# Optimization experiments

Measured on AMD Instinct MI355X. Metric: run time of the kernel, lower is better.

Reference implementation:

```python
import jax, jax.numpy as jnp
import numpy as np

B, S, DM1, DM2, DK, DV = 8, 2048, 768, 768, 64, 64
EPS = 1e-5


def setup_inputs() -> dict:
    key = jax.random.key(0)
    ks = jax.random.split(key, 8)
    s1 = 1.0 / np.sqrt(DM1)
    s2 = 1.0 / np.sqrt(DM2)
    return {
        "x_1": jax.random.normal(ks[0], (B, S, DM1), jnp.float32),
        "x_2": jax.random.normal(ks[1], (B, S, DM2), jnp.float32),
        "Wq": jax.random.uniform(ks[2], (DM1, DK), jnp.float32, -s1, s1),
        "bq": jnp.zeros((DK,), jnp.float32),
        "Wk": jax.random.uniform(ks[3], (DM2, DK), jnp.float32, -s2, s2),
        "bk": jnp.zeros((DK,), jnp.float32),
        "Wv": jax.random.uniform(ks[4], (DM2, DV), jnp.float32, -s2, s2),
        "bv": jnp.zeros((DV,), jnp.float32),
        "gamma": jnp.ones((DV,), jnp.float32),
        "beta": jnp.zeros((DV,), jnp.float32),
    }


def reference(x_1, x_2, Wq, bq, Wk, bk, Wv, bv, gamma, beta):
    q = jnp.einsum("bsd,dk->bsk", x_1, Wq) + bq            # [B,S,DK]
    k = jnp.einsum("bsd,dk->bsk", x_2, Wk) + bk            # [B,S,DK]
    v = jnp.einsum("bsd,dv->bsv", x_2, Wv) + bv            # [B,S,DV]
    scores = jnp.einsum("bqk,bsk->bqs", q, k) / jnp.sqrt(jnp.float32(DK))
    w = jax.nn.softmax(scores, axis=-1)                    # [B,S,S]
    # reverse-weight transform (reverse=True)
    dim = w.shape[1]
    w = (1.0 - w) / (dim - 1)
    attn = jnp.einsum("bqs,bsv->bqv", w, v)                # [B,S,DV]
    mu = jnp.mean(attn, axis=-1, keepdims=True)
    var = jnp.var(attn, axis=-1, keepdims=True)
    out = (attn - mu) * jax.lax.rsqrt(var + EPS) * gamma + beta
    return out
```

## Files before the change

kernel.cpp:

```cpp
#include <hip/hip_runtime.h>
#include <hip/hip_bf16.h>

#define BATCH 8
#define SEQ   2048
#define DM    768
#define DD    64
#define BS (BATCH * SEQ)
#define SCALEQ 0.1803369380478f

typedef __bf16 bf16x8 __attribute__((ext_vector_type(8)));
typedef float  f32x4  __attribute__((ext_vector_type(4)));
typedef short  short8 __attribute__((ext_vector_type(8)));
typedef short  short4v __attribute__((ext_vector_type(4)));

#define MFMA16(a, b, c) __builtin_amdgcn_mfma_f32_16x16x32_bf16((a), (b), (c), 0, 0, 0)

__device__ __forceinline__ short f2bf(float x) {
    unsigned u = __builtin_bit_cast(unsigned, x);
    u = (u + 0x7fffu + ((u >> 16) & 1u)) >> 16;
    return (short)u;
}
__device__ __forceinline__ float bf2f(short s) {
    unsigned u = ((unsigned)(unsigned short)s) << 16;
    return __builtin_bit_cast(float, u);
}
__device__ __forceinline__ bf16x8 cvt8(float4 a, float4 b) {
    bf16x8 r;
    r[0] = (__bf16)a.x; r[1] = (__bf16)a.y; r[2] = (__bf16)a.z; r[3] = (__bf16)a.w;
    r[4] = (__bf16)b.x; r[5] = (__bf16)b.y; r[6] = (__bf16)b.z; r[7] = (__bf16)b.w;
    return r;
}

__global__ void prep_w_kernel(const float* __restrict__ Wq, const float* __restrict__ Wk,
                              const float* __restrict__ Wv, short* __restrict__ Wt,
                              float* __restrict__ C) {
    int idx = blockIdx.x * 256 + threadIdx.x;
    if (idx < BATCH * DD) C[idx] = 0.f;
    if (idx >= 3 * DM * DD) return;
    int m = idx / (DM * DD);
    int r = (idx % (DM * DD)) / DD;
    int c = idx % DD;
    const float* W = (m == 0) ? Wq : (m == 1) ? Wk : Wv;
    float scale = (m == 0) ? SCALEQ : 1.0f;
    Wt[m * DM * DD + c * DM + r] = f2bf(W[r * DD + c] * scale);
}

#define PHK 192
#define RSTR 200
__global__ __launch_bounds__(256) void proj_kernel(
        const float* __restrict__ x1, const float* __restrict__ x2,
        const short* __restrict__ Wt,
        const float* __restrict__ bq, const float* __restrict__ bk,
        const float* __restrict__ bv,
        short* __restrict__ Qs, short* __restrict__ Kb, short* __restrict__ Vtb,
        float* __restrict__ C) {
    __shared__ __align__(16) short wls[2][64 * RSTR];
    const int tid = threadIdx.x, wave = tid >> 6, lane = tid & 63;
    const int quad = lane >> 4, l15 = lane & 15;
    const int kv = blockIdx.x & 1;
    const int r0 = (blockIdx.x >> 1) * 64;
    const float* x = kv ? x2 : x1;
    const short* W0 = Wt + (kv ? (size_t)(DM * DD) : 0);
    const short* W1 = Wt + 2 * (size_t)(DM * DD);

    const int srow = tid >> 2;
    const int skseg = tid & 3;

    const float* xp = x + (size_t)(r0 + wave * 16 + l15) * DM + quad * 8;

    f32x4 acc0[4] = {}, acc1[4] = {};

    float4 cxa = *(const float4*)(xp);
    float4 cxb = *(const float4*)(xp + 4);

    for (int ph = 0; ph < 4; ph++) {
        const int kbase = ph * PHK;
#pragma unroll
        for (int i = 0; i < 6; i++) {
            int kp = skseg + 4 * i;
            bf16x8 w = *(const bf16x8*)(W0 + (size_t)srow * DM + kbase + kp * 8);
            *(bf16x8*)&wls[0][srow * RSTR + kp * 8] = w;
        }
        if (kv) {
#pragma unroll
            for (int i = 0; i < 6; i++) {
                int kp = skseg + 4 * i;
                bf16x8 w = *(const bf16x8*)(W1 + (size_t)srow * DM + kbase + kp * 8);
                *(bf16x8*)&wls[1][srow * RSTR + kp * 8] = w;
            }
        }
        __syncthreads();
#pragma unroll
        for (int st = 0; st < 6; st++) {
            const int k0 = kbase + st * 32;
            float4 nxa, nxb;
            if (k0 + 32 < DM) {
                nxa = *(const float4*)(xp + k0 + 32);
                nxb = *(const float4*)(xp + k0 + 36);
            }
            bf16x8 af = cvt8(cxa, cxb);
#pragma unroll
            for (int tn = 0; tn < 4; tn++) {
                const int lofs = (tn * 16 + l15) * RSTR + (st * 4 + quad) * 8;
                acc0[tn] = MFMA16(af, *(const bf16x8*)&wls[0][lofs], acc0[tn]);
                if (kv)
                    acc1[tn] = MFMA16(af, *(const bf16x8*)&wls[1][lofs], acc1[tn]);
            }
            cxa = nxa; cxb = nxb;
        }
        __syncthreads();
    }

    if (!kv) {
#pragma unroll
        for (int tn = 0; tn < 4; tn++) {
            int v = tn * 16 + l15;
            float bb = bq[v] * SCALEQ;
#pragma unroll
            for (int r = 0; r < 4; r++)
                Qs[(size_t)(r0 + wave * 16 + quad * 4 + r) * DD + v] = f2bf(acc0[tn][r] + bb);
        }
    } else {
#pragma unroll
        for (int tn = 0; tn < 4; tn++) {
            int v = tn * 16 + l15;
            float bb = bk[v];
#pragma unroll
            for (int r = 0; r < 4; r++)
                Kb[(size_t)(r0 + wave * 16 + quad * 4 + r) * DD + v] = f2bf(acc0[tn][r] + bb);
        }
        const int b = r0 / SEQ;
        const int sbase = (r0 % SEQ) + wave * 16 + quad * 4;
#pragma unroll
        for (int tn = 0; tn < 4; tn++) {
            int v = tn * 16 + l15;
            float bb = bv[v];
            short4v pk;
            float cs = 0.f;
#pragma unroll
            for (int r = 0; r < 4; r++) {
                pk[r] = f2bf(acc1[tn][r] + bb);
                cs += bf2f(pk[r]);
            }
            *(short4v*)(Vtb + ((size_t)b * DD + v) * SEQ + sbase) = pk;
            cs += __shfl_xor(cs, 16);
            cs += __shfl_xor(cs, 32);
            if (quad == 0) atomicAdd(&C[b * DD + v], cs);
        }
    }
}

#define PBS 72
__global__ __launch_bounds__(256, 2) void flash_kernel(
        const short* __restrict__ Q, const short* __restrict__ K,
        const short* __restrict__ Vt,
        short* __restrict__ Yp, float* __restrict__ Dp) {
    __shared__ __align__(16) short pbuf[4][64 * PBS];
    __shared__ float dl[4][64];
    const int tid  = threadIdx.x;
    const int wave = tid >> 6, lane = tid & 63, quad = lane >> 4, l15 = lane & 15;
    const int blk = blockIdx.x;
    const int b = blk & 7, qt = (blk >> 3) & 31, half = blk >> 8;
    const int q0 = qt * 64;

    bf16x8 qf[4][2];
#pragma unroll
    for (int qn = 0; qn < 4; qn++)
#pragma unroll
        for (int kc = 0; kc < 2; kc++)
            qf[qn][kc] = *(const bf16x8*)(Q + ((size_t)(b * SEQ + q0 + qn * 16 + l15)) * DD
                                          + kc * 32 + quad * 8);

    const short* Kbp = K  + (size_t)b * SEQ * DD;
    const short* Vbp = Vt + (size_t)b * DD * SEQ;
    f32x4 y[4][4] = {};
    float den[4] = {0.f, 0.f, 0.f, 0.f};
    short* pw = &pbuf[wave][0];

    const int s_begin = half * 1024 + wave * 256;
    for (int s0 = s_begin; s0 < s_begin + 256; s0 += 64) {
#pragma unroll
        for (int tn = 0; tn < 4; tn++) {
            const short* kf = Kbp + (size_t)(s0 + tn * 16 + l15) * DD + quad * 8;
            bf16x8 ka0 = *(const bf16x8*)kf;
            bf16x8 ka1 = *(const bf16x8*)(kf + 32);
#pragma unroll
            for (int qn = 0; qn < 4; qn++) {
                f32x4 z = {0.f, 0.f, 0.f, 0.f};
                z = MFMA16(ka0, qf[qn][0], z);
                z = MFMA16(ka1, qf[qn][1], z);
                short4v pk;
#pragma unroll
                for (int r = 0; r < 4; r++) {
                    float p = __builtin_amdgcn_exp2f(z[r]);
                    den[qn] += p;
                    pk[r] = f2bf(p);
                }
                *(short4v*)&pw[(qn * 16 + l15) * PBS + tn * 16 + quad * 4] = pk;
            }
        }
#pragma unroll
        for (int kc = 0; kc < 2; kc++) {
            bf16x8 pB[4];
#pragma unroll
            for (int qn = 0; qn < 4; qn++)
                pB[qn] = *(const bf16x8*)&pw[(qn * 16 + l15) * PBS + kc * 32 + quad * 8];
#pragma unroll
            for (int vn = 0; vn < 4; vn++) {
                bf16x8 va = *(const bf16x8*)(Vbp + (size_t)(vn * 16 + l15) * SEQ
                                             + s0 + kc * 32 + quad * 8);
#pragma unroll
                for (int qn = 0; qn < 4; qn++)
                    y[qn][vn] = MFMA16(va, pB[qn], y[qn][vn]);
            }
        }
    }
#pragma unroll
    for (int qn = 0; qn < 4; qn++) {
        den[qn] += __shfl_xor(den[qn], 16);
        den[qn] += __shfl_xor(den[qn], 32);
    }
#pragma unroll
    for (int qn = 0; qn < 4; qn++) {
#pragma unroll
        for (int vn = 0; vn < 4; vn++) {
            short4v pk;
#pragma unroll
            for (int r = 0; r < 4; r++) pk[r] = f2bf(y[qn][vn][r]);
            *(short4v*)&pw[(qn * 16 + l15) * PBS + vn * 16 + quad * 4] = pk;
        }
        if (quad == 0) dl[wave][qn * 16 + l15] = den[qn];
    }
    __syncthreads();
    {
        const int q = wave * 16 + l15;
        float D = dl[0][q] + dl[1][q] + dl[2][q] + dl[3][q];
        float ys[16];
#pragma unroll
        for (int j = 0; j < 16; j++) ys[j] = 0.f;
#pragma unroll
        for (int u = 0; u < 4; u++) {
#pragma unroll
            for (int h = 0; h < 2; h++) {
                bf16x8 t = *(const bf16x8*)&pbuf[u][q * PBS + quad * 16 + h * 8];
#pragma unroll
                for (int j = 0; j < 8; j++) ys[h * 8 + j] += (float)t[j];
            }
        }
        const size_t row = (size_t)b * SEQ + q0 + q;
        short8 o0, o1;
#pragma unroll
        for (int j = 0; j < 8; j++) { o0[j] = f2bf(ys[j]); o1[j] = f2bf(ys[8 + j]); }
        short* yout = Yp + ((size_t)half * BS + row) * DD + quad * 16;
        *(short8*)yout = o0;
        *(short8*)(yout + 8) = o1;
        if (quad == 0) Dp[half * BS + row] = D;
    }
}

__global__ __launch_bounds__(256) void reduce_ln_kernel(
        const short* __restrict__ Yp, const float* __restrict__ Dp,
        const float* __restrict__ C, const float* __restrict__ gamma,
        const float* __restrict__ beta, float* __restrict__ out) {
    const int row = blockIdx.x * 4 + (threadIdx.x >> 6);
    const int v = threadIdx.x & 63;
    const int b = row >> 11;
    float Y = bf2f(Yp[(size_t)row * DD + v]) + bf2f(Yp[((size_t)BS + row) * DD + v]);
    float D = Dp[row] + Dp[BS + row];
    float attn = (C[b * DD + v] - Y / D) * (1.0f / (float)(SEQ - 1));
    float msum = attn, ssum = attn * attn;
#pragma unroll
    for (int m = 1; m < 64; m <<= 1) {
        msum += __shfl_xor(msum, m);
        ssum += __shfl_xor(ssum, m);
    }
    float mu = msum * (1.0f / 64.0f);
    float var = ssum * (1.0f / 64.0f) - mu * mu;
    float rs = rsqrtf(var + 1e-5f);
    out[(size_t)row * DD + v] = (attn - mu) * rs * gamma[v] + beta[v];
}

extern "C" void kernel_launch(void* const* d_in, const int* in_sizes, int n_in,
                              void* d_out, int out_size, void* d_ws, size_t ws_size,
                              hipStream_t stream) {
    const float* x1    = (const float*)d_in[0];
    const float* x2    = (const float*)d_in[1];
    const float* Wq    = (const float*)d_in[2];
    const float* bq    = (const float*)d_in[3];
    const float* Wk    = (const float*)d_in[4];
    const float* bk    = (const float*)d_in[5];
    const float* Wv    = (const float*)d_in[6];
    const float* bv    = (const float*)d_in[7];
    const float* gamma = (const float*)d_in[8];
    const float* beta  = (const float*)d_in[9];
    float* out = (float*)d_out;

    char* ws = (char*)d_ws;
    short* Qs  = (short*)(ws);
    short* Kbf = (short*)(ws + (2ull << 20));
    short* Vtb = (short*)(ws + (4ull << 20));
    short* Wt  = (short*)(ws + (6ull << 20));
    float* Cc  = (float*)(ws + (6ull << 20) + 3 * DM * DD * 2);
    short* Yp  = (short*)(ws + (7ull << 20));
    float* Dp  = (float*)(ws + (11ull << 20));

    prep_w_kernel<<<576, 256, 0, stream>>>(Wq, Wk, Wv, Wt, Cc);
    proj_kernel<<<512, 256, 0, stream>>>(x1, x2, Wt, bq, bk, bv, Qs, Kbf, Vtb, Cc);
    flash_kernel<<<512, 256, 0, stream>>>(Qs, Kbf, Vtb, Yp, Dp);
    reduce_ln_kernel<<<BS / 4, 256, 0, stream>>>(Yp, Dp, Cc, gamma, beta, out);
}
```

Baseline: 170.4 us.

## Read projection weights directly from global memory instead of staging through LDS

The projection kernel no longer copies weight tiles into shared memory with barriers. Each lane now loads its bf16 weight fragments straight from global memory, relying on L1/L2 caching since all blocks share the same small weight matrices. The K loop is fully unrolled per branch, and launch bounds request two blocks per SM. This removes LDS traffic and __syncthreads, at the cost of more global/cache loads per MFMA and higher register pressure from the unroll. It also drops the explicit software prefetch of x.

```diff
diff --git a/kernel.cpp b/kernel.cpp
--- a/kernel.cpp
+++ b/kernel.cpp
@@ -45,16 +45,13 @@
     Wt[m * DM * DD + c * DM + r] = f2bf(W[r * DD + c] * scale);
 }
 
-#define PHK 192
-#define RSTR 200
-__global__ __launch_bounds__(256) void proj_kernel(
+__global__ __launch_bounds__(256, 2) void proj_kernel(
         const float* __restrict__ x1, const float* __restrict__ x2,
         const short* __restrict__ Wt,
         const float* __restrict__ bq, const float* __restrict__ bk,
         const float* __restrict__ bv,
         short* __restrict__ Qs, short* __restrict__ Kb, short* __restrict__ Vtb,
         float* __restrict__ C) {
-    __shared__ __align__(16) short wls[2][64 * RSTR];
     const int tid = threadIdx.x, wave = tid >> 6, lane = tid & 63;
     const int quad = lane >> 4, l15 = lane & 15;
     const int kv = blockIdx.x & 1;
@@ -63,55 +60,28 @@
     const short* W0 = Wt + (kv ? (size_t)(DM * DD) : 0);
     const short* W1 = Wt + 2 * (size_t)(DM * DD);
 
-    const int srow = tid >> 2;
-    const int skseg = tid & 3;
-
     const float* xp = x + (size_t)(r0 + wave * 16 + l15) * DM + quad * 8;
+    const short* wp0[4];
+    const short* wp1[4];
+#pragma unroll
+    for (int tn = 0; tn < 4; tn++) {
+        wp0[tn] = W0 + (size_t)(tn * 16 + l15) * DM + quad * 8;
+        wp1[tn] = W1 + (size_t)(tn * 16 + l15) * DM + quad * 8;
+    }
 
     f32x4 acc0[4] = {}, acc1[4] = {};
 
-    float4 cxa = *(const float4*)(xp);
-    float4 cxb = *(const float4*)(xp + 4);
-
-    for (int ph = 0; ph < 4; ph++) {
-        const int kbase = ph * PHK;
-#pragma unroll
-        for (int i = 0; i < 6; i++) {
-            int kp = skseg + 4 * i;
-            bf16x8 w = *(const bf16x8*)(W0 + (size_t)srow * DM + kbase + kp * 8);
-            *(bf16x8*)&wls[0][srow * RSTR + kp * 8] = w;
-        }
-        if (kv) {
-#pragma unroll
-            for (int i = 0; i < 6; i++) {
-                int kp = skseg + 4 * i;
-                bf16x8 w = *(const bf16x8*)(W1 + (size_t)srow * DM + kbase + kp * 8);
-                *(bf16x8*)&wls[1][srow * RSTR + kp * 8] = w;
-            }
-        }
-        __syncthreads();
-#pragma unroll
-        for (int st = 0; st < 6; st++) {
-            const int k0 = kbase + st * 32;
-            float4 nxa, nxb;
-            if (k0 + 32 < DM) {
-                nxa = *(const float4*)(xp + k0 + 32);
-                nxb = *(const float4*)(xp + k0 + 36);
-            }
-            bf16x8 af = cvt8(cxa, cxb);
-#pragma unroll
-            for (int tn = 0; tn < 4; tn++) {
-                const int lofs = (tn * 16 + l15) * RSTR + (st * 4 + quad) * 8;
-                acc0[tn] = MFMA16(af, *(const bf16x8*)&wls[0][lofs], acc0[tn]);
-                if (kv)
-                    acc1[tn] = MFMA16(af, *(const bf16x8*)&wls[1][lofs], acc1[tn]);
-            }
-            cxa = nxa; cxb = nxb;
-        }
-        __syncthreads();
-    }
-
     if (!kv) {
+#pragma unroll
+        for (int st = 0; st < 24; st++) {
+            const int k0 = st * 32;
+            float4 a = *(const float4*)(xp + k0);
+            float4 b = *(const float4*)(xp + k0 + 4);
+            bf16x8 af = cvt8(a, b);
+#pragma unroll
+            for (int tn = 0; tn < 4; tn++)
+                acc0[tn] = MFMA16(af, *(const bf16x8*)(wp0[tn] + k0), acc0[tn]);
+        }
 #pragma unroll
         for (int tn = 0; tn < 4; tn++) {
             int v = tn * 16 + l15;
@@ -121,6 +91,18 @@
                 Qs[(size_t)(r0 + wave * 16 + quad * 4 + r) * DD + v] = f2bf(acc0[tn][r] + bb);
         }
     } else {
+#pragma unroll
+        for (int st = 0; st < 24; st++) {
+            const int k0 = st * 32;
+            float4 a = *(const float4*)(xp + k0);
+            float4 b = *(const float4*)(xp + k0 + 4);
+            bf16x8 af = cvt8(a, b);
+#pragma unroll
+            for (int tn = 0; tn < 4; tn++) {
+                acc0[tn] = MFMA16(af, *(const bf16x8*)(wp0[tn] + k0), acc0[tn]);
+                acc1[tn] = MFMA16(af, *(const bf16x8*)(wp1[tn] + k0), acc1[tn]);
+            }
+        }
 #pragma unroll
         for (int tn = 0; tn < 4; tn++) {
             int v = tn * 16 + l15;
```

New measurement: 203.6 us. 1.19x slower.

## Split K/V projection into separate blocks and hoist flash-kernel global loads

Applied to the files above, without the earlier changes.

The projection kernel now launches 768 blocks, each computing a single projection (Q, K, or V) over 64 rows, instead of 512 blocks where K/V blocks did double work. This balances per-block load and halves LDS use per block, at the cost of reading x2 twice. In the flash kernel, K and V fragment loads are batched ahead of their MFMA loops, with sched_barriers to issue memory early and hide latency, at the cost of more registers.

```diff
diff --git a/kernel.cpp b/kernel.cpp
--- a/kernel.cpp
+++ b/kernel.cpp
@@ -54,21 +54,28 @@
         const float* __restrict__ bv,
         short* __restrict__ Qs, short* __restrict__ Kb, short* __restrict__ Vtb,
         float* __restrict__ C) {
-    __shared__ __align__(16) short wls[2][64 * RSTR];
+    __shared__ __align__(16) short wls[64 * RSTR];
     const int tid = threadIdx.x, wave = tid >> 6, lane = tid & 63;
     const int quad = lane >> 4, l15 = lane & 15;
-    const int kv = blockIdx.x & 1;
-    const int r0 = (blockIdx.x >> 1) * 64;
-    const float* x = kv ? x2 : x1;
-    const short* W0 = Wt + (kv ? (size_t)(DM * DD) : 0);
-    const short* W1 = Wt + 2 * (size_t)(DM * DD);
+    const int blk = blockIdx.x;
+    int typ, g;
+    if (blk < 512) {
+        typ = 1 + ((blk & 15) >> 3);
+        g = ((blk >> 4) << 3) | (blk & 7);
+    } else {
+        typ = 0;
+        g = blk - 512;
+    }
+    const int r0 = g * 64;
+    const float* x = typ ? x2 : x1;
+    const short* W0 = Wt + (size_t)typ * DM * DD;
 
     const int srow = tid >> 2;
     const int skseg = tid & 3;
 
     const float* xp = x + (size_t)(r0 + wave * 16 + l15) * DM + quad * 8;
 
-    f32x4 acc0[4] = {}, acc1[4] = {};
+    f32x4 acc[4] = {};
 
     float4 cxa = *(const float4*)(xp);
     float4 cxb = *(const float4*)(xp + 4);
@@ -79,15 +86,7 @@
         for (int i = 0; i < 6; i++) {
             int kp = skseg + 4 * i;
             bf16x8 w = *(const bf16x8*)(W0 + (size_t)srow * DM + kbase + kp * 8);
-            *(bf16x8*)&wls[0][srow * RSTR + kp * 8] = w;
-        }
-        if (kv) {
-#pragma unroll
-            for (int i = 0; i < 6; i++) {
-                int kp = skseg + 4 * i;
-                bf16x8 w = *(const bf16x8*)(W1 + (size_t)srow * DM + kbase + kp * 8);
-                *(bf16x8*)&wls[1][srow * RSTR + kp * 8] = w;
-            }
+            *(bf16x8*)&wls[srow * RSTR + kp * 8] = w;
         }
         __syncthreads();
 #pragma unroll
@@ -102,33 +101,32 @@
 #pragma unroll
             for (int tn = 0; tn < 4; tn++) {
                 const int lofs = (tn * 16 + l15) * RSTR + (st * 4 + quad) * 8;
-                acc0[tn] = MFMA16(af, *(const bf16x8*)&wls[0][lofs], acc0[tn]);
-                if (kv)
-                    acc1[tn] = MFMA16(af, *(const bf16x8*)&wls[1][lofs], acc1[tn]);
+                acc[tn] = MFMA16(af, *(const bf16x8*)&wls[lofs], acc[tn]);
             }
             cxa = nxa; cxb = nxb;
         }
         __syncthreads();
     }
 
-    if (!kv) {
+    if (typ == 0) {
 #pragma unroll
         for (int tn = 0; tn < 4; tn++) {
             int v = tn * 16 + l15;
             float bb = bq[v] * SCALEQ;
 #pragma unroll
             for (int r = 0; r < 4; r++)
-                Qs[(size_t)(r0 + wave * 16 + quad * 4 + r) * DD + v] = f2bf(acc0[tn][r] + bb);
-        }
-    } else {
+                Qs[(size_t)(r0 + wave * 16 + quad * 4 + r) * DD + v] = f2bf(acc[tn][r] + bb);
+        }
+    } else if (typ == 1) {
 #pragma unroll
         for (int tn = 0; tn < 4; tn++) {
             int v = tn * 16 + l15;
             float bb = bk[v];
 #pragma unroll
             for (int r = 0; r < 4; r++)
-                Kb[(size_t)(r0 + wave * 16 + quad * 4 + r) * DD + v] = f2bf(acc0[tn][r] + bb);
-        }
+                Kb[(size_t)(r0 + wave * 16 + quad * 4 + r) * DD + v] = f2bf(acc[tn][r] + bb);
+        }
+    } else {
         const int b = r0 / SEQ;
         const int sbase = (r0 % SEQ) + wave * 16 + quad * 4;
 #pragma unroll
@@ -139,7 +137,7 @@
             float cs = 0.f;
 #pragma unroll
             for (int r = 0; r < 4; r++) {
-                pk[r] = f2bf(acc1[tn][r] + bb);
+                pk[r] = f2bf(acc[tn][r] + bb);
                 cs += bf2f(pk[r]);
             }
             *(short4v*)(Vtb + ((size_t)b * DD + v) * SEQ + sbase) = pk;
@@ -179,16 +177,21 @@
 
     const int s_begin = half * 1024 + wave * 256;
     for (int s0 = s_begin; s0 < s_begin + 256; s0 += 64) {
+        bf16x8 ka[4][2];
 #pragma unroll
         for (int tn = 0; tn < 4; tn++) {
             const short* kf = Kbp + (size_t)(s0 + tn * 16 + l15) * DD + quad * 8;
-            bf16x8 ka0 = *(const bf16x8*)kf;
-            bf16x8 ka1 = *(const bf16x8*)(kf + 32);
+            ka[tn][0] = *(const bf16x8*)kf;
+            ka[tn][1] = *(const bf16x8*)(kf + 32);
+        }
+        __builtin_amdgcn_sched_barrier(0);
+#pragma unroll
+        for (int tn = 0; tn < 4; tn++) {
 #pragma unroll
             for (int qn = 0; qn < 4; qn++) {
                 f32x4 z = {0.f, 0.f, 0.f, 0.f};
-                z = MFMA16(ka0, qf[qn][0], z);
-                z = MFMA16(ka1, qf[qn][1], z);
+                z = MFMA16(ka[tn][0], qf[qn][0], z);
+                z = MFMA16(ka[tn][1], qf[qn][1], z);
                 short4v pk;
 #pragma unroll
                 for (int r = 0; r < 4; r++) {
@@ -199,6 +202,14 @@
                 *(short4v*)&pw[(qn * 16 + l15) * PBS + tn * 16 + quad * 4] = pk;
             }
         }
+        bf16x8 va[2][4];
+#pragma unroll
+        for (int kc = 0; kc < 2; kc++)
+#pragma unroll
+            for (int vn = 0; vn < 4; vn++)
+                va[kc][vn] = *(const bf16x8*)(Vbp + (size_t)(vn * 16 + l15) * SEQ
+                                              + s0 + kc * 32 + quad * 8);
+        __builtin_amdgcn_sched_barrier(0);
 #pragma unroll
         for (int kc = 0; kc < 2; kc++) {
             bf16x8 pB[4];
@@ -207,11 +218,9 @@
                 pB[qn] = *(const bf16x8*)&pw[(qn * 16 + l15) * PBS + kc * 32 + quad * 8];
 #pragma unroll
             for (int vn = 0; vn < 4; vn++) {
-                bf16x8 va = *(const bf16x8*)(Vbp + (size_t)(vn * 16 + l15) * SEQ
-                                             + s0 + kc * 32 + quad * 8);
 #pragma unroll
                 for (int qn = 0; qn < 4; qn++)
-                    y[qn][vn] = MFMA16(va, pB[qn], y[qn][vn]);
+                    y[qn][vn] = MFMA16(va[kc][vn], pB[qn], y[qn][vn]);
             }
         }
     }
@@ -305,7 +314,7 @@
     float* Dp  = (float*)(ws + (11ull << 20));
 
     prep_w_kernel<<<576, 256, 0, stream>>>(Wq, Wk, Wv, Wt, Cc);
-    proj_kernel<<<512, 256, 0, stream>>>(x1, x2, Wt, bq, bk, bv, Qs, Kbf, Vtb, Cc);
+    proj_kernel<<<768, 256, 0, stream>>>(x1, x2, Wt, bq, bk, bv, Qs, Kbf, Vtb, Cc);
     flash_kernel<<<512, 256, 0, stream>>>(Qs, Kbf, Vtb, Yp, Dp);
     reduce_ln_kernel<<<BS / 4, 256, 0, stream>>>(Yp, Dp, Cc, gamma, beta, out);
 }
```

New measurement: 174.4 us. +2.3%, slower.
